# Optimization experiments

Hardware: AMD Instinct MI355X
Metric: run time of the kernel (lower is better)

The kernel has to match this reference:

```python
import jax, jax.numpy as jnp
import numpy as np

EPS = 1e-5
C_M, C, C_Z = 256, 32, 128
N_SEQ, N_RES = 256, 1024


def setup_inputs() -> dict:
    key = jax.random.key(0)
    k1, k2, k3 = jax.random.split(key, 3)
    msa = jax.random.normal(k1, (N_SEQ, N_RES, C_M), dtype=jnp.float32)
    norm_w = jnp.ones((C_M,), dtype=jnp.float32)
    norm_b = jnp.zeros((C_M,), dtype=jnp.float32)
    w_ab = jax.random.normal(k2, (C, C_M), dtype=jnp.float32) * (1.0 / np.sqrt(C_M))
    b_ab = jnp.zeros((C,), dtype=jnp.float32)
    w_out = jax.random.normal(k3, (C_Z, C * C), dtype=jnp.float32) * (1.0 / C)
    b_out = jnp.zeros((C_Z,), dtype=jnp.float32)
    return {"msa": msa, "norm_w": norm_w, "norm_b": norm_b,
            "w_ab": w_ab, "b_ab": b_ab, "w_out": w_out, "b_out": b_out}


def reference(msa, norm_w, norm_b, w_ab, b_ab, w_out, b_out):
    # msa: (s, r, c_m) -> (r, s, c_m)
    x = jnp.transpose(msa, (1, 0, 2))
    s = x.shape[1]
    # LayerNorm over c_m
    mu = jnp.mean(x, axis=-1, keepdims=True)
    var = jnp.mean(jnp.square(x - mu), axis=-1, keepdims=True)
    xn = (x - mu) * jax.lax.rsqrt(var + EPS) * norm_w + norm_b
    # a == b: same linear applied twice to same input in the original
    a = jnp.einsum('rsm,cm->rsc', xn, w_ab) + b_ab          # (r, s, c)
    # mean over s of outer product == batched A^T A / s  -> (r, c, c)
    o = jnp.einsum('rsx,rsy->rxy', a, a) / s
    o = o.reshape(o.shape[0], C * C)                        # (r, c*c)
    pre_pair = jnp.einsum('rk,zk->rz', o, w_out) + b_out    # (r, c_z)
    r = pre_pair.shape[0]
    # unsqueeze(1).expand(r, r, c_z)
    pair = jnp.broadcast_to(pre_pair[:, None, :], (r, r, C_Z))
    return pair
```

## Files before the change

kernel.cpp:

```cpp
#include <hip/hip_runtime.h>

#define NSEQ 256
#define NRES 1024
#define CM   256
#define CC   32
#define CZ   128
#define EPS  1e-5f
#define SROW (NRES * CM)

__launch_bounds__(256, 4)
__global__ void opm_fused(const float* __restrict__ msa,
                          const float* __restrict__ nw,
                          const float* __restrict__ nb,
                          const float* __restrict__ w_ab,
                          const float* __restrict__ b_ab,
                          const float* __restrict__ w_out,
                          const float* __restrict__ b_out,
                          float* __restrict__ out)
{
    __shared__ float buf[CM * CC];
    __shared__ float K1[CC], K2[CC];
    __shared__ float o_lds[CC * CC];
    __shared__ float pre_part[2 * CZ];
    __shared__ float pre_lds[CZ];

    const int tid = threadIdx.x;
    const int r   = blockIdx.x;

    {
        const int c  = tid & 31;
        const int m0 = tid >> 5;
        #pragma unroll
        for (int k = 0; k < 32; ++k) {
            const int m = m0 + (k << 3);
            buf[m * CC + c] = nw[m] * w_ab[c * CM + m];
        }
    }
    __syncthreads();
    if (tid < CC) {
        const int c = tid;
        float k1 = 0.f, k2 = 0.f;
        for (int m = 0; m < CM; ++m) {
            k1 += buf[m * CC + c];
            k2 = fmaf(nb[m], w_ab[c * CM + m], k2);
        }
        K1[c] = k1;
        K2[c] = k2 + b_ab[c];
    }
    __syncthreads();

    const int sc = tid & 7;
    const int sg = tid >> 3;
    const int c0 = sc * 4;
    const float* xr = msa + (size_t)r * CM;

    float G[8][4];
    float ssum[8], ssq[8];
    #pragma unroll
    for (int j = 0; j < 8; ++j) {
        ssum[j] = 0.f; ssq[j] = 0.f;
        #pragma unroll
        for (int cc = 0; cc < 4; ++cc) G[j][cc] = 0.f;
    }

    const float* xrow[8];
    #pragma unroll
    for (int j = 0; j < 8; ++j)
        xrow[j] = xr + (size_t)(sg + (j << 5)) * SROW;

    for (int mb = 0; mb < CM; mb += 4) {
        const float4 w0 = *(const float4*)&buf[(mb + 0) * CC + c0];
        const float4 w1 = *(const float4*)&buf[(mb + 1) * CC + c0];
        const float4 w2 = *(const float4*)&buf[(mb + 2) * CC + c0];
        const float4 w3 = *(const float4*)&buf[(mb + 3) * CC + c0];
        float4 xv[8];
        #pragma unroll
        for (int j = 0; j < 8; ++j)
            xv[j] = *(const float4*)(xrow[j] + mb);
        #pragma unroll
        for (int j = 0; j < 8; ++j) {
            const float4 x4 = xv[j];
            G[j][0] = fmaf(x4.x, w0.x, fmaf(x4.y, w1.x, fmaf(x4.z, w2.x, fmaf(x4.w, w3.x, G[j][0]))));
            G[j][1] = fmaf(x4.x, w0.y, fmaf(x4.y, w1.y, fmaf(x4.z, w2.y, fmaf(x4.w, w3.y, G[j][1]))));
            G[j][2] = fmaf(x4.x, w0.z, fmaf(x4.y, w1.z, fmaf(x4.z, w2.z, fmaf(x4.w, w3.z, G[j][2]))));
            G[j][3] = fmaf(x4.x, w0.w, fmaf(x4.y, w1.w, fmaf(x4.z, w2.w, fmaf(x4.w, w3.w, G[j][3]))));
            ssum[j] += (x4.x + x4.y) + (x4.z + x4.w);
            ssq[j]  = fmaf(x4.x, x4.x, fmaf(x4.y, x4.y, fmaf(x4.z, x4.z, fmaf(x4.w, x4.w, ssq[j]))));
        }
    }

    float a_reg[8][4];
    {
        const float k1a = K1[c0 + 0], k1b = K1[c0 + 1], k1c = K1[c0 + 2], k1d = K1[c0 + 3];
        const float k2a = K2[c0 + 0], k2b = K2[c0 + 1], k2c = K2[c0 + 2], k2d = K2[c0 + 3];
        #pragma unroll
        for (int j = 0; j < 8; ++j) {
            const float mu   = ssum[j] * (1.f / CM);
            const float var  = ssq[j] * (1.f / CM) - mu * mu;
            const float rstd = 1.f / sqrtf(var + EPS);
            a_reg[j][0] = fmaf(rstd, G[j][0] - mu * k1a, k2a);
            a_reg[j][1] = fmaf(rstd, G[j][1] - mu * k1b, k2b);
            a_reg[j][2] = fmaf(rstd, G[j][2] - mu * k1c, k2c);
            a_reg[j][3] = fmaf(rstd, G[j][3] - mu * k1d, k2d);
        }
    }
    __syncthreads();
    #pragma unroll
    for (int j = 0; j < 8; ++j) {
        const int s = sg + (j << 5);
        *(float4*)&buf[s * CC + c0] =
            make_float4(a_reg[j][0], a_reg[j][1], a_reg[j][2], a_reg[j][3]);
    }
    __syncthreads();

    const int xi = (tid >> 4) << 1;
    const int yi = (tid & 15) << 1;
    float o00 = 0.f, o01 = 0.f, o10 = 0.f, o11 = 0.f;
    #pragma unroll 4
    for (int s = 0; s < NSEQ; ++s) {
        const float2 ax = *(const float2*)&buf[s * CC + xi];
        const float2 ay = *(const float2*)&buf[s * CC + yi];
        o00 = fmaf(ax.x, ay.x, o00);
        o01 = fmaf(ax.x, ay.y, o01);
        o10 = fmaf(ax.y, ay.x, o10);
        o11 = fmaf(ax.y, ay.y, o11);
    }
    {
        const float inv_s = 1.f / NSEQ;
        *(float2*)&o_lds[xi * CC + yi]       = make_float2(o00 * inv_s, o01 * inv_s);
        *(float2*)&o_lds[(xi + 1) * CC + yi] = make_float2(o10 * inv_s, o11 * inv_s);
    }
    __syncthreads();

    {
        const int z    = tid & 127;
        const int half = tid >> 7;
        const float* wrow = w_out + (size_t)z * (CC * CC) + half * 512;
        const float* op   = o_lds + half * 512;
        float po = 0.f;
        for (int k = 0; k < 512; k += 4) {
            const float4 o4 = *(const float4*)&op[k];
            const float4 w4 = *(const float4*)&wrow[k];
            po = fmaf(o4.x, w4.x, fmaf(o4.y, w4.y, fmaf(o4.z, w4.z, fmaf(o4.w, w4.w, po))));
        }
        pre_part[half * CZ + z] = po;
    }
    __syncthreads();
    if (tid < CZ) pre_lds[tid] = pre_part[tid] + pre_part[CZ + tid] + b_out[tid];
    __syncthreads();

    {
        const int z4 = tid & 31;
        const int jo = tid >> 5;
        const float4 pv = *(const float4*)&pre_lds[z4 * 4];
        float4* outp = (float4*)out + (size_t)r * NRES * (CZ / 4);
        for (int j0 = 0; j0 < NRES; j0 += 8) {
            outp[(size_t)(j0 + jo) * (CZ / 4) + z4] = pv;
        }
    }
}

extern "C" void kernel_launch(void* const* d_in, const int* in_sizes, int n_in,
                              void* d_out, int out_size, void* d_ws, size_t ws_size,
                              hipStream_t stream) {
    const float* msa   = (const float*)d_in[0];
    const float* nw    = (const float*)d_in[1];
    const float* nb    = (const float*)d_in[2];
    const float* w_ab  = (const float*)d_in[3];
    const float* b_ab  = (const float*)d_in[4];
    const float* w_out = (const float*)d_in[5];
    const float* b_out = (const float*)d_in[6];
    float* out = (float*)d_out;

    opm_fused<<<NRES, 256, 0, stream>>>(msa, nw, nb, w_ab, b_ab, w_out, b_out, out);
}
```

Baseline: 975.4 us.

## Stage MSA chunks through padded LDS with register prefetch and nontemporal output stores

Replaces the strided per-thread global float4 loads of MSA rows with coalesced loads of 32-column chunks into a padded LDS tile, prefetching the next chunk into registers while computing on the current one. The K1/K2 reduction is parallelised across all threads, the w_out loop is unrolled, and the large broadcast output write uses nontemporal stores. This adds about 36KB of LDS and lowers launch bounds to 2 waves per EU, which may reduce occupancy.

```diff
diff --git a/kernel.cpp b/kernel.cpp
--- a/kernel.cpp
+++ b/kernel.cpp
@@ -7,8 +7,12 @@
 #define CZ   128
 #define EPS  1e-5f
 #define SROW (NRES * CM)
-
-__launch_bounds__(256, 4)
+#define MCH  32
+#define XPAD 36
+
+typedef float f4v __attribute__((ext_vector_type(4)));
+
+__launch_bounds__(256, 2)
 __global__ void opm_fused(const float* __restrict__ msa,
                           const float* __restrict__ nw,
                           const float* __restrict__ nb,
@@ -18,9 +22,11 @@
                           const float* __restrict__ b_out,
                           float* __restrict__ out)
 {
-    __shared__ float buf[CM * CC];
+    __shared__ float wt[CM * CC];
+    __shared__ float xt[NSEQ * XPAD];
+    __shared__ float o_lds[CC * CC];
+    __shared__ float K1p[8 * CC], K2p[8 * CC];
     __shared__ float K1[CC], K2[CC];
-    __shared__ float o_lds[CC * CC];
     __shared__ float pre_part[2 * CZ];
     __shared__ float pre_lds[CZ];
 
@@ -33,21 +39,31 @@
         #pragma unroll
         for (int k = 0; k < 32; ++k) {
             const int m = m0 + (k << 3);
-            buf[m * CC + c] = nw[m] * w_ab[c * CM + m];
-        }
+            wt[m * CC + c] = nw[m] * w_ab[c * CM + m];
+        }
+    }
+    __syncthreads();
+    {
+        const int c    = tid & 31;
+        const int part = tid >> 5;
+        float k1 = 0.f, k2 = 0.f;
+        #pragma unroll 8
+        for (int i = 0; i < 32; ++i) {
+            const int m = part * 32 + i;
+            k1 += wt[m * CC + c];
+            k2 = fmaf(nb[m], w_ab[c * CM + m], k2);
+        }
+        K1p[part * CC + c] = k1;
+        K2p[part * CC + c] = k2;
     }
     __syncthreads();
     if (tid < CC) {
-        const int c = tid;
         float k1 = 0.f, k2 = 0.f;
-        for (int m = 0; m < CM; ++m) {
-            k1 += buf[m * CC + c];
-            k2 = fmaf(nb[m], w_ab[c * CM + m], k2);
-        }
-        K1[c] = k1;
-        K2[c] = k2 + b_ab[c];
-    }
-    __syncthreads();
+        #pragma unroll
+        for (int p = 0; p < 8; ++p) { k1 += K1p[p * CC + tid]; k2 += K2p[p * CC + tid]; }
+        K1[tid] = k1;
+        K2[tid] = k2 + b_ab[tid];
+    }
 
     const int sc = tid & 7;
     const int sg = tid >> 3;
@@ -63,29 +79,38 @@
         for (int cc = 0; cc < 4; ++cc) G[j][cc] = 0.f;
     }
 
-    const float* xrow[8];
+    float4 pf[8];
     #pragma unroll
-    for (int j = 0; j < 8; ++j)
-        xrow[j] = xr + (size_t)(sg + (j << 5)) * SROW;
-
-    for (int mb = 0; mb < CM; mb += 4) {
-        const float4 w0 = *(const float4*)&buf[(mb + 0) * CC + c0];
-        const float4 w1 = *(const float4*)&buf[(mb + 1) * CC + c0];
-        const float4 w2 = *(const float4*)&buf[(mb + 2) * CC + c0];
-        const float4 w3 = *(const float4*)&buf[(mb + 3) * CC + c0];
-        float4 xv[8];
-        #pragma unroll
-        for (int j = 0; j < 8; ++j)
-            xv[j] = *(const float4*)(xrow[j] + mb);
-        #pragma unroll
-        for (int j = 0; j < 8; ++j) {
-            const float4 x4 = xv[j];
-            G[j][0] = fmaf(x4.x, w0.x, fmaf(x4.y, w1.x, fmaf(x4.z, w2.x, fmaf(x4.w, w3.x, G[j][0]))));
-            G[j][1] = fmaf(x4.x, w0.y, fmaf(x4.y, w1.y, fmaf(x4.z, w2.y, fmaf(x4.w, w3.y, G[j][1]))));
-            G[j][2] = fmaf(x4.x, w0.z, fmaf(x4.y, w1.z, fmaf(x4.z, w2.z, fmaf(x4.w, w3.z, G[j][2]))));
-            G[j][3] = fmaf(x4.x, w0.w, fmaf(x4.y, w1.w, fmaf(x4.z, w2.w, fmaf(x4.w, w3.w, G[j][3]))));
-            ssum[j] += (x4.x + x4.y) + (x4.z + x4.w);
-            ssq[j]  = fmaf(x4.x, x4.x, fmaf(x4.y, x4.y, fmaf(x4.z, x4.z, fmaf(x4.w, x4.w, ssq[j]))));
+    for (int k = 0; k < 8; ++k)
+        pf[k] = *(const float4*)(xr + (size_t)(sg + (k << 5)) * SROW + (sc << 2));
+
+    for (int mb = 0; mb < CM; mb += MCH) {
+        __syncthreads();
+        #pragma unroll
+        for (int k = 0; k < 8; ++k)
+            *(float4*)&xt[(sg + (k << 5)) * XPAD + (sc << 2)] = pf[k];
+        __syncthreads();
+        if (mb + MCH < CM) {
+            #pragma unroll
+            for (int k = 0; k < 8; ++k)
+                pf[k] = *(const float4*)(xr + (size_t)(sg + (k << 5)) * SROW + (mb + MCH) + (sc << 2));
+        }
+        #pragma unroll
+        for (int mm = 0; mm < MCH; mm += 4) {
+            const float4 w0 = *(const float4*)&wt[(mb + mm + 0) * CC + c0];
+            const float4 w1 = *(const float4*)&wt[(mb + mm + 1) * CC + c0];
+            const float4 w2 = *(const float4*)&wt[(mb + mm + 2) * CC + c0];
+            const float4 w3 = *(const float4*)&wt[(mb + mm + 3) * CC + c0];
+            #pragma unroll
+            for (int j = 0; j < 8; ++j) {
+                const float4 x4 = *(const float4*)&xt[(sg + (j << 5)) * XPAD + mm];
+                G[j][0] = fmaf(x4.x, w0.x, fmaf(x4.y, w1.x, fmaf(x4.z, w2.x, fmaf(x4.w, w3.x, G[j][0]))));
+                G[j][1] = fmaf(x4.x, w0.y, fmaf(x4.y, w1.y, fmaf(x4.z, w2.y, fmaf(x4.w, w3.y, G[j][1]))));
+                G[j][2] = fmaf(x4.x, w0.z, fmaf(x4.y, w1.z, fmaf(x4.z, w2.z, fmaf(x4.w, w3.z, G[j][2]))));
+                G[j][3] = fmaf(x4.x, w0.w, fmaf(x4.y, w1.w, fmaf(x4.z, w2.w, fmaf(x4.w, w3.w, G[j][3]))));
+                ssum[j] += (x4.x + x4.y) + (x4.z + x4.w);
+                ssq[j]  = fmaf(x4.x, x4.x, fmaf(x4.y, x4.y, fmaf(x4.z, x4.z, fmaf(x4.w, x4.w, ssq[j]))));
+            }
         }
     }
 
@@ -108,7 +133,7 @@
     #pragma unroll
     for (int j = 0; j < 8; ++j) {
         const int s = sg + (j << 5);
-        *(float4*)&buf[s * CC + c0] =
+        *(float4*)&xt[s * CC + c0] =
             make_float4(a_reg[j][0], a_reg[j][1], a_reg[j][2], a_reg[j][3]);
     }
     __syncthreads();
@@ -118,8 +143,8 @@
     float o00 = 0.f, o01 = 0.f, o10 = 0.f, o11 = 0.f;
     #pragma unroll 4
     for (int s = 0; s < NSEQ; ++s) {
-        const float2 ax = *(const float2*)&buf[s * CC + xi];
-        const float2 ay = *(const float2*)&buf[s * CC + yi];
+        const float2 ax = *(const float2*)&xt[s * CC + xi];
+        const float2 ay = *(const float2*)&xt[s * CC + yi];
         o00 = fmaf(ax.x, ay.x, o00);
         o01 = fmaf(ax.x, ay.y, o01);
         o10 = fmaf(ax.y, ay.x, o10);
@@ -138,6 +163,7 @@
         const float* wrow = w_out + (size_t)z * (CC * CC) + half * 512;
         const float* op   = o_lds + half * 512;
         float po = 0.f;
+        #pragma unroll 8
         for (int k = 0; k < 512; k += 4) {
             const float4 o4 = *(const float4*)&op[k];
             const float4 w4 = *(const float4*)&wrow[k];
@@ -152,10 +178,14 @@
     {
         const int z4 = tid & 31;
         const int jo = tid >> 5;
-        const float4 pv = *(const float4*)&pre_lds[z4 * 4];
-        float4* outp = (float4*)out + (size_t)r * NRES * (CZ / 4);
+        f4v pv;
+        pv.x = pre_lds[z4 * 4 + 0];
+        pv.y = pre_lds[z4 * 4 + 1];
+        pv.z = pre_lds[z4 * 4 + 2];
+        pv.w = pre_lds[z4 * 4 + 3];
+        f4v* outp = (f4v*)out + (size_t)r * NRES * (CZ / 4);
         for (int j0 = 0; j0 < NRES; j0 += 8) {
-            outp[(size_t)(j0 + jo) * (CZ / 4) + z4] = pv;
+            __builtin_nontemporal_store(pv, &outp[(size_t)(j0 + jo) * (CZ / 4) + z4]);
         }
     }
 }
```

After: 840.3 us. 1.16x faster.
